# Optimization experiments

Hardware: AMD Instinct MI355X
Metric: run time of the kernel (lower is better)

Reference implementation:

```python
import jax, jax.numpy as jnp
import numpy as np
import math

N_REL = 53
OUT_C = 230
FEAT = 3 * OUT_C  # 690
B = 512
S_MAX = 128
NEG_INF = -1e30


def setup_inputs() -> dict:
    key = jax.random.key(0)
    k1, k2, k3, k4 = jax.random.split(key, 4)
    features = jax.random.normal(k1, (B, S_MAX, FEAT), dtype=jnp.float32)
    # variable bag sizes (>=1 so every softmax row has at least one valid sentence)
    lengths = jax.random.randint(k2, (B,), 1, S_MAX + 1, dtype=jnp.int32)
    con = math.sqrt(6.0 / (FEAT + N_REL))
    r_embed = jax.random.uniform(k3, (N_REL, FEAT), dtype=jnp.float32, minval=-con, maxval=con)
    r_bias = jax.random.uniform(k4, (N_REL,), dtype=jnp.float32, minval=-con, maxval=con)
    # att_W initialized as identity expanded over relations (as in the torch module)
    att_W = jnp.broadcast_to(jnp.eye(FEAT, dtype=jnp.float32), (N_REL, FEAT, FEAT)).copy()
    return {"features": features, "lengths": lengths, "r_embed": r_embed,
            "r_bias": r_bias, "att_W": att_W}


def reference(features, lengths, r_embed, r_bias, att_W):
    # features: [B, S, F] padded sentence features per bag; lengths: [B]
    Bn, S, Fd = features.shape
    valid = jnp.arange(S)[None, :] < lengths[:, None]          # [B, S]
    # attention logits: r_embed[r] @ att_W[r] @ feature[s]
    m = jnp.einsum('rf,rfg->rg', r_embed, att_W)               # [R, F]
    logits = jnp.einsum('rg,bsg->brs', m, features)            # [B, R, S]
    logits = jnp.where(valid[:, None, :], logits, NEG_INF)
    w = jax.nn.softmax(logits, axis=-1)                        # per-bag attention over sentences
    s = jnp.einsum('brs,bsf->brf', w, features)                # [B, R, F]
    s = s * 0.5                                                # eval-mode dropout scaling in source
    scores = jnp.einsum('brf,kf->brk', s, r_embed) + r_bias    # [B, R, R]
    pred = jax.nn.log_softmax(scores, axis=-1).max(axis=1)     # [B, R] (eval path)
    return pred
```

## Files before the change

### kernel.cpp

```cpp
#include <hip/hip_runtime.h>

#define NREL 53
#define FEAT 690
#define NBAGS 512
#define SMAX 128
#define K2 106
#define KPAD 704
#define NT 22
#define LDSTR 40

typedef short bf16x8 __attribute__((ext_vector_type(8)));
typedef short short4v __attribute__((ext_vector_type(4)));
typedef short short8v __attribute__((ext_vector_type(8)));
typedef float f32x4 __attribute__((ext_vector_type(4)));

__device__ __forceinline__ short f2bf(float x) {
    union { float f; unsigned u; } c; c.f = x;
    unsigned r = c.u + 0x7fffu + ((c.u >> 16) & 1u);
    return (short)(r >> 16);
}

#define FCH 30
__global__ __launch_bounds__(256) void k_m(const float* __restrict__ r_embed,
                                           const float* __restrict__ att_W,
                                           float* __restrict__ m_ws) {
    const int gc = blockIdx.x, fc = blockIdx.y, r = blockIdx.z;
    const int g = gc * 512 + threadIdx.x * 2;
    const int f0 = fc * FCH;
    __shared__ float re[FCH];
    if (threadIdx.x < FCH) re[threadIdx.x] = r_embed[r * FEAT + f0 + threadIdx.x];
    __syncthreads();
    if (g >= FEAT) return;
    const float* aw = att_W + (size_t)r * FEAT * FEAT + (size_t)f0 * FEAT + g;
    float ax = 0.f, ay = 0.f;
    #pragma unroll
    for (int j = 0; j < FCH; ++j) {
        const float2 t = *(const float2*)&aw[(size_t)j * FEAT];
        ax += re[j] * t.x;
        ay += re[j] * t.y;
    }
    atomicAdd(&m_ws[r * FEAT + g], ax);
    atomicAdd(&m_ws[r * FEAT + g + 1], ay);
}

__global__ __launch_bounds__(256) void k_prep(const float* __restrict__ m_ws,
                                              const float* __restrict__ r_embed,
                                              short* __restrict__ Bws) {
    const int n = blockIdx.x;
    for (int f = threadIdx.x; f < KPAD; f += 256) {
        float v = 0.f;
        if (f < FEAT) {
            if (n < NREL)    v = m_ws[n * FEAT + f];
            else if (n < K2) v = r_embed[(n - NREL) * FEAT + f];
        }
        Bws[n * KPAD + f] = f2bf(v);
    }
}

__global__ __launch_bounds__(256) void k_proj(const float* __restrict__ features,
                                              const int* __restrict__ lengths,
                                              const short* __restrict__ Bws,
                                              float* __restrict__ projT) {
    const int b = blockIdx.x;
    const int L = lengths[b];
    __shared__ short Ash[2][128 * LDSTR];
    __shared__ short Bsh[2][128 * LDSTR];
    const int tid = threadIdx.x;
    const int wave = tid >> 6, lane = tid & 63;
    const int wr = (wave >> 1) * 64, wc = (wave & 1) * 64;
    const int r16 = lane & 15, g = lane >> 4;
    const float* fb = features + (size_t)b * SMAX * FEAT;

    f32x4 acc[4][4];
    #pragma unroll
    for (int m = 0; m < 4; ++m)
        #pragma unroll
        for (int n = 0; n < 4; ++n) acc[m][n] = (f32x4)0.f;

    const int srow = tid >> 3;
    const int fo   = (tid & 7) * 4;
    const int bn   = tid >> 2;
    const int bc   = (tid & 3) * 8;

    {
        #pragma unroll
        for (int it = 0; it < 4; ++it) {
            if (it * 32 < L) {
                const int s = it * 32 + srow;
                const float* p = fb + (size_t)s * FEAT + fo;
                const float2 v0 = *(const float2*)p;
                const float2 v1 = *(const float2*)(p + 2);
                short4v w = {f2bf(v0.x), f2bf(v0.y), f2bf(v1.x), f2bf(v1.y)};
                *(short4v*)&Ash[0][s * LDSTR + fo] = w;
            }
        }
        #pragma unroll
        for (int jt = 0; jt < 2; ++jt) {
            const int n = jt * 64 + bn;
            *(short8v*)&Bsh[0][n * LDSTR + bc] =
                *(const short8v*)&Bws[n * KPAD + bc];
        }
    }
    __syncthreads();

    int cur = 0;
    for (int kt = 0; kt < NT; ++kt) {
        const bool have_next = (kt + 1 < NT);
        float2 av[4][2];
        short8v bv[2];
        if (have_next) {
            const int k0n = (kt + 1) * 32;
            const bool lastn = (kt + 1 == NT - 1);
            #pragma unroll
            for (int it = 0; it < 4; ++it) {
                if (it * 32 < L) {
                    const int s = it * 32 + srow;
                    const int f0 = k0n + fo;
                    const float* p = fb + (size_t)s * FEAT + f0;
                    if (!lastn) {
                        av[it][0] = *(const float2*)p;
                        av[it][1] = *(const float2*)(p + 2);
                    } else {
                        av[it][0] = (f0 + 1 < FEAT) ? *(const float2*)p       : make_float2(0.f, 0.f);
                        av[it][1] = (f0 + 3 < FEAT) ? *(const float2*)(p + 2) : make_float2(0.f, 0.f);
                    }
                }
            }
            #pragma unroll
            for (int jt = 0; jt < 2; ++jt) {
                const int n = jt * 64 + bn;
                bv[jt] = *(const short8v*)&Bws[n * KPAD + k0n + bc];
            }
        }

        if (wr < L) {
            const short* Ab = &Ash[cur][0];
            const short* Bb = &Bsh[cur][0];
            bf16x8 af[4], bfv[4];
            #pragma unroll
            for (int m = 0; m < 4; ++m)
                af[m] = *(const bf16x8*)&Ab[(wr + m * 16 + r16) * LDSTR + g * 8];
            #pragma unroll
            for (int n = 0; n < 4; ++n)
                bfv[n] = *(const bf16x8*)&Bb[(wc + n * 16 + r16) * LDSTR + g * 8];
            #pragma unroll
            for (int m = 0; m < 4; ++m)
                #pragma unroll
                for (int n = 0; n < 4; ++n)
                    acc[m][n] = __builtin_amdgcn_mfma_f32_16x16x32_bf16(af[m], bfv[n], acc[m][n], 0, 0, 0);
        }

        if (have_next) {
            #pragma unroll
            for (int it = 0; it < 4; ++it) {
                if (it * 32 < L) {
                    const int s = it * 32 + srow;
                    short4v w = {f2bf(av[it][0].x), f2bf(av[it][0].y),
                                 f2bf(av[it][1].x), f2bf(av[it][1].y)};
                    *(short4v*)&Ash[cur ^ 1][s * LDSTR + fo] = w;
                }
            }
            #pragma unroll
            for (int jt = 0; jt < 2; ++jt) {
                const int n = jt * 64 + bn;
                *(short8v*)&Bsh[cur ^ 1][n * LDSTR + bc] = bv[jt];
            }
        }
        __syncthreads();
        cur ^= 1;
    }

    if (wr < L) {
        float* pT = projT + (size_t)b * K2 * SMAX;
        #pragma unroll
        for (int m = 0; m < 4; ++m) {
            const int s0 = wr + m * 16 + g * 4;
            if (s0 < L) {
                #pragma unroll
                for (int n = 0; n < 4; ++n) {
                    const int k = wc + n * 16 + r16;
                    if (k < K2) *(f32x4*)&pT[k * SMAX + s0] = acc[m][n];
                }
            }
        }
    }
}

__global__ __launch_bounds__(256) void k_finish(const float* __restrict__ projT,
                                                const int* __restrict__ lengths,
                                                const float* __restrict__ r_bias,
                                                float* __restrict__ out) {
    const int b = blockIdx.x;
    const int L = lengths[b];
    __shared__ float wS[SMAX * 61];
    __shared__ float pRs[SMAX * 61];
    __shared__ float sc[NREL * 56];
    __shared__ float lse[NREL];
    const int tid = threadIdx.x;
    const int wv = tid >> 6, lane = tid & 63;
    const float* pb = projT + (size_t)b * K2 * SMAX;

    for (int idx = tid; idx < NREL * SMAX; idx += 256) {
        const int k = idx >> 7, s = idx & 127;
        pRs[s * 61 + k] = pb[(size_t)(NREL + k) * SMAX + s];
    }
    for (int r = wv; r < NREL; r += 4) {
        const float* row = pb + (size_t)r * SMAX;
        float v0 = (lane < L)      ? row[lane]      : -1e30f;
        float v1 = (lane + 64 < L) ? row[lane + 64] : -1e30f;
        float mx = fmaxf(v0, v1);
        for (int o = 32; o; o >>= 1) mx = fmaxf(mx, __shfl_xor(mx, o));
        float e0 = (lane < L)      ? __expf(v0 - mx) : 0.f;
        float e1 = (lane + 64 < L) ? __expf(v1 - mx) : 0.f;
        float sm = e0 + e1;
        for (int o = 32; o; o >>= 1) sm += __shfl_xor(sm, o);
        const float inv = 0.5f / sm;
        if (lane < L)      wS[lane * 61 + r]        = e0 * inv;
        if (lane + 64 < L) wS[(lane + 64) * 61 + r] = e1 * inv;
    }
    __syncthreads();

    {
        const int ty = tid >> 4, tx = tid & 15;
        if (ty < 14 && tx < 14) {
            const int rr = ty * 4, kk = tx * 4;
            float a4[4][4] = {};
            for (int s = 0; s < L; ++s) {
                float aa[4], bb[4];
                #pragma unroll
                for (int i = 0; i < 4; ++i) aa[i] = wS[s * 61 + rr + i];
                #pragma unroll
                for (int n = 0; n < 4; ++n) bb[n] = pRs[s * 61 + kk + n];
                #pragma unroll
                for (int i = 0; i < 4; ++i)
                    #pragma unroll
                    for (int n = 0; n < 4; ++n) a4[i][n] += aa[i] * bb[n];
            }
            #pragma unroll
            for (int i = 0; i < 4; ++i) {
                const int r = rr + i;
                if (r < NREL) {
                    #pragma unroll
                    for (int n = 0; n < 4; ++n) {
                        const int k = kk + n;
                        if (k < NREL) sc[r * 56 + k] = a4[i][n] + r_bias[k];
                    }
                }
            }
        }
    }
    __syncthreads();

    for (int r = wv; r < NREL; r += 4) {
        const float v = (lane < NREL) ? sc[r * 56 + lane] : -1e30f;
        float mx = v;
        for (int o = 32; o; o >>= 1) mx = fmaxf(mx, __shfl_xor(mx, o));
        float e = (lane < NREL) ? __expf(v - mx) : 0.f;
        for (int o = 32; o; o >>= 1) e += __shfl_xor(e, o);
        if (lane == 0) lse[r] = mx + __logf(e);
    }
    __syncthreads();

    if (tid < NREL) {
        float best = -1e30f;
        for (int r = 0; r < NREL; ++r) best = fmaxf(best, sc[r * 56 + tid] - lse[r]);
        out[b * NREL + tid] = best;
    }
}

extern "C" void kernel_launch(void* const* d_in, const int* in_sizes, int n_in,
                              void* d_out, int out_size, void* d_ws, size_t ws_size,
                              hipStream_t stream) {
    const float* features = (const float*)d_in[0];
    const int*   lengths  = (const int*)d_in[1];
    const float* r_embed  = (const float*)d_in[2];
    const float* r_bias   = (const float*)d_in[3];
    const float* att_W    = (const float*)d_in[4];
    float* out = (float*)d_out;

    float* m_ws  = (float*)d_ws;
    short* Bws   = (short*)((char*)d_ws + (1 << 18));
    float* projT = (float*)((char*)d_ws + (1 << 19));

    hipMemsetAsync(m_ws, 0, NREL * FEAT * sizeof(float), stream);

    dim3 g1(2, 23, NREL);
    k_m<<<g1, 256, 0, stream>>>(r_embed, att_W, m_ws);
    k_prep<<<128, 256, 0, stream>>>(m_ws, r_embed, Bws);
    k_proj<<<NBAGS, 256, 0, stream>>>(features, lengths, Bws, projT);
    k_finish<<<NBAGS, 256, 0, stream>>>(projT, lengths, r_bias, out);
}
```

Measured before the change: 363.0 us.

## Load projection B operand directly to registers and vectorize finish-kernel LDS layout

```diff
diff --git a/kernel.cpp b/kernel.cpp
--- a/kernel.cpp
+++ b/kernel.cpp
@@ -1,4 +1,5 @@
 #include <hip/hip_runtime.h>
+#include <hip/hip_bf16.h>
 
 #define NREL 53
 #define FEAT 690
@@ -8,6 +9,7 @@
 #define KPAD 704
 #define NT 22
 #define LDSTR 40
+#define WSTR 140
 
 typedef short bf16x8 __attribute__((ext_vector_type(8)));
 typedef short short4v __attribute__((ext_vector_type(4)));
@@ -18,6 +20,15 @@
     union { float f; unsigned u; } c; c.f = x;
     unsigned r = c.u + 0x7fffu + ((c.u >> 16) & 1u);
     return (short)(r >> 16);
+}
+
+__device__ __forceinline__ short4v pack4(float a, float b, float c, float d) {
+    __hip_bfloat162 p0 = __float22bfloat162_rn(make_float2(a, b));
+    __hip_bfloat162 p1 = __float22bfloat162_rn(make_float2(c, d));
+    union { __hip_bfloat162 h; short2 s; } u0, u1;
+    u0.h = p0; u1.h = p1;
+    short4v w = {u0.s.x, u0.s.y, u1.s.x, u1.s.y};
+    return w;
 }
 
 #define FCH 30
@@ -64,12 +75,12 @@
     const int b = blockIdx.x;
     const int L = lengths[b];
     __shared__ short Ash[2][128 * LDSTR];
-    __shared__ short Bsh[2][128 * LDSTR];
     const int tid = threadIdx.x;
     const int wave = tid >> 6, lane = tid & 63;
     const int wr = (wave >> 1) * 64, wc = (wave & 1) * 64;
     const int r16 = lane & 15, g = lane >> 4;
     const float* fb = features + (size_t)b * SMAX * FEAT;
+    const bool active = (wr < L);
 
     f32x4 acc[4][4];
     #pragma unroll
@@ -79,27 +90,21 @@
 
     const int srow = tid >> 3;
     const int fo   = (tid & 7) * 4;
-    const int bn   = tid >> 2;
-    const int bc   = (tid & 3) * 8;
-
-    {
+
+    #pragma unroll
+    for (int it = 0; it < 4; ++it) {
+        if (it * 32 < L) {
+            const int s = it * 32 + srow;
+            const float2 v0 = *(const float2*)&fb[(size_t)s * FEAT + fo];
+            const float2 v1 = *(const float2*)&fb[(size_t)s * FEAT + fo + 2];
+            *(short4v*)&Ash[0][s * LDSTR + fo] = pack4(v0.x, v0.y, v1.x, v1.y);
+        }
+    }
+    short8v bcur[4], bnext[4];
+    if (active) {
         #pragma unroll
-        for (int it = 0; it < 4; ++it) {
-            if (it * 32 < L) {
-                const int s = it * 32 + srow;
-                const float* p = fb + (size_t)s * FEAT + fo;
-                const float2 v0 = *(const float2*)p;
-                const float2 v1 = *(const float2*)(p + 2);
-                short4v w = {f2bf(v0.x), f2bf(v0.y), f2bf(v1.x), f2bf(v1.y)};
-                *(short4v*)&Ash[0][s * LDSTR + fo] = w;
-            }
-        }
-        #pragma unroll
-        for (int jt = 0; jt < 2; ++jt) {
-            const int n = jt * 64 + bn;
-            *(short8v*)&Bsh[0][n * LDSTR + bc] =
-                *(const short8v*)&Bws[n * KPAD + bc];
-        }
+        for (int n = 0; n < 4; ++n)
+            bcur[n] = *(const short8v*)&Bws[(size_t)(wc + n * 16 + r16) * KPAD + g * 8];
     }
     __syncthreads();
 
@@ -107,7 +112,6 @@
     for (int kt = 0; kt < NT; ++kt) {
         const bool have_next = (kt + 1 < NT);
         float2 av[4][2];
-        short8v bv[2];
         if (have_next) {
             const int k0n = (kt + 1) * 32;
             const bool lastn = (kt + 1 == NT - 1);
@@ -126,28 +130,23 @@
                     }
                 }
             }
-            #pragma unroll
-            for (int jt = 0; jt < 2; ++jt) {
-                const int n = jt * 64 + bn;
-                bv[jt] = *(const short8v*)&Bws[n * KPAD + k0n + bc];
-            }
-        }
-
-        if (wr < L) {
-            const short* Ab = &Ash[cur][0];
-            const short* Bb = &Bsh[cur][0];
-            bf16x8 af[4], bfv[4];
+            if (active) {
+                #pragma unroll
+                for (int n = 0; n < 4; ++n)
+                    bnext[n] = *(const short8v*)&Bws[(size_t)(wc + n * 16 + r16) * KPAD + k0n + g * 8];
+            }
+        }
+
+        if (active) {
+            bf16x8 af[4];
             #pragma unroll
             for (int m = 0; m < 4; ++m)
-                af[m] = *(const bf16x8*)&Ab[(wr + m * 16 + r16) * LDSTR + g * 8];
-            #pragma unroll
-            for (int n = 0; n < 4; ++n)
-                bfv[n] = *(const bf16x8*)&Bb[(wc + n * 16 + r16) * LDSTR + g * 8];
+                af[m] = *(const bf16x8*)&Ash[cur][(wr + m * 16 + r16) * LDSTR + g * 8];
             #pragma unroll
             for (int m = 0; m < 4; ++m)
                 #pragma unroll
                 for (int n = 0; n < 4; ++n)
-                    acc[m][n] = __builtin_amdgcn_mfma_f32_16x16x32_bf16(af[m], bfv[n], acc[m][n], 0, 0, 0);
+                    acc[m][n] = __builtin_amdgcn_mfma_f32_16x16x32_bf16(af[m], (bf16x8)bcur[n], acc[m][n], 0, 0, 0);
         }
 
         if (have_next) {
@@ -155,22 +154,20 @@
             for (int it = 0; it < 4; ++it) {
                 if (it * 32 < L) {
                     const int s = it * 32 + srow;
-                    short4v w = {f2bf(av[it][0].x), f2bf(av[it][0].y),
-                                 f2bf(av[it][1].x), f2bf(av[it][1].y)};
-                    *(short4v*)&Ash[cur ^ 1][s * LDSTR + fo] = w;
-                }
-            }
-            #pragma unroll
-            for (int jt = 0; jt < 2; ++jt) {
-                const int n = jt * 64 + bn;
-                *(short8v*)&Bsh[cur ^ 1][n * LDSTR + bc] = bv[jt];
+                    *(short4v*)&Ash[cur ^ 1][s * LDSTR + fo] =
+                        pack4(av[it][0].x, av[it][0].y, av[it][1].x, av[it][1].y);
+                }
+            }
+            if (active) {
+                #pragma unroll
+                for (int n = 0; n < 4; ++n) bcur[n] = bnext[n];
             }
         }
         __syncthreads();
         cur ^= 1;
     }
 
-    if (wr < L) {
+    if (active) {
         float* pT = projT + (size_t)b * K2 * SMAX;
         #pragma unroll
         for (int m = 0; m < 4; ++m) {
@@ -192,17 +189,18 @@
                                                 float* __restrict__ out) {
     const int b = blockIdx.x;
     const int L = lengths[b];
-    __shared__ float wS[SMAX * 61];
-    __shared__ float pRs[SMAX * 61];
+    const int Lp = ((L + 3) >> 2) << 2;
+    __shared__ float wS[56 * WSTR];
+    __shared__ float pRs[56 * WSTR];
     __shared__ float sc[NREL * 56];
     __shared__ float lse[NREL];
     const int tid = threadIdx.x;
     const int wv = tid >> 6, lane = tid & 63;
     const float* pb = projT + (size_t)b * K2 * SMAX;
 
-    for (int idx = tid; idx < NREL * SMAX; idx += 256) {
-        const int k = idx >> 7, s = idx & 127;
-        pRs[s * 61 + k] = pb[(size_t)(NREL + k) * SMAX + s];
+    for (int idx = tid; idx < NREL * 32; idx += 256) {
+        const int k = idx >> 5, s4 = (idx & 31) * 4;
+        *(float4*)&pRs[k * WSTR + s4] = *(const float4*)&pb[(size_t)(NREL + k) * SMAX + s4];
     }
     for (int r = wv; r < NREL; r += 4) {
         const float* row = pb + (size_t)r * SMAX;
@@ -215,8 +213,8 @@
         float sm = e0 + e1;
         for (int o = 32; o; o >>= 1) sm += __shfl_xor(sm, o);
         const float inv = 0.5f / sm;
-        if (lane < L)      wS[lane * 61 + r]        = e0 * inv;
-        if (lane + 64 < L) wS[(lane + 64) * 61 + r] = e1 * inv;
+        if (lane < Lp)      wS[r * WSTR + lane]      = e0 * inv;
+        if (lane + 64 < Lp) wS[r * WSTR + lane + 64] = e1 * inv;
     }
     __syncthreads();
 
@@ -225,16 +223,18 @@
         if (ty < 14 && tx < 14) {
             const int rr = ty * 4, kk = tx * 4;
             float a4[4][4] = {};
-            for (int s = 0; s < L; ++s) {
-                float aa[4], bb[4];
-                #pragma unroll
-                for (int i = 0; i < 4; ++i) aa[i] = wS[s * 61 + rr + i];
-                #pragma unroll
-                for (int n = 0; n < 4; ++n) bb[n] = pRs[s * 61 + kk + n];
+            for (int s = 0; s < Lp; s += 4) {
+                float4 aa[4], bb[4];
+                #pragma unroll
+                for (int i = 0; i < 4; ++i) aa[i] = *(const float4*)&wS[(rr + i) * WSTR + s];
+                #pragma unroll
+                for (int n = 0; n < 4; ++n) bb[n] = *(const float4*)&pRs[(kk + n) * WSTR + s];
                 #pragma unroll
                 for (int i = 0; i < 4; ++i)
                     #pragma unroll
-                    for (int n = 0; n < 4; ++n) a4[i][n] += aa[i] * bb[n];
+                    for (int n = 0; n < 4; ++n)
+                        a4[i][n] += aa[i].x * bb[n].x + aa[i].y * bb[n].y
+                                  + aa[i].z * bb[n].z + aa[i].w * bb[n].w;
             }
             #pragma unroll
             for (int i = 0; i < 4; ++i) {
```

After: 389.8 us. 7.4% more time.
